# Optimization experiments

Hardware: AMD Instinct MI355X
Metric: run time of the kernel (lower is better)

## Reference

```python
import jax, jax.numpy as jnp
import numpy as np

E, M, K, I, TOPK = 8, 4096, 2048, 1408, 2
N = 2 * I  # gated: w1 produces [gate, up]


def setup_inputs() -> dict:
    key = jax.random.key(0)
    k1, k2, k3, k4, k5 = jax.random.split(key, 5)
    hidden_states = jax.random.normal(k1, (M, K), dtype=jnp.float32)
    w1 = jax.random.normal(k2, (E, N, K), dtype=jnp.float32) * 0.02
    w2 = jax.random.normal(k3, (E, K, I), dtype=jnp.float32) * 0.02
    raw = jax.random.uniform(k4, (M, TOPK), dtype=jnp.float32)
    topk_weights = raw / jnp.sum(raw, axis=-1, keepdims=True)  # router probs
    topk_ids = jax.random.randint(k5, (M, TOPK), 0, E, dtype=jnp.int32)
    return {
        "hidden_states": hidden_states,
        "w1": w1,
        "w2": w2,
        "topk_weights": topk_weights,
        "topk_ids": topk_ids,
    }


def reference(hidden_states, w1, w2, topk_weights, topk_ids):
    # MoE: permute -> grouped GEMM1 -> silu_and_mul -> grouped GEMM2 -> unpermute+reduce.
    # Dense-per-expert formulation (math-equivalent to grouped GEMM over routed tokens).
    # GEMM1: [E, M, N]
    h1 = jnp.einsum("mk,enk->emn", hidden_states, w1)
    gate, up = h1[..., :I], h1[..., I:]
    act = jax.nn.silu(gate) * up  # silu_and_mul, [E, M, I]
    # GEMM2: [E, M, K]
    y = jnp.einsum("emi,eki->emk", act, w2)
    # Unpermute: gather each token's topk expert outputs, apply router weights, reduce.
    y_tok = jnp.transpose(y, (1, 0, 2))  # [M, E, K]
    sel = jnp.take_along_axis(y_tok, topk_ids[:, :, None].astype(jnp.int32), axis=1)  # [M, topk, K]
    out = jnp.sum(sel * topk_weights[:, :, None], axis=1)  # [M, K]
    return out
```

## Files before the change

### kernel.cpp

```cpp
#include <hip/hip_runtime.h>
#include <hip/hip_bf16.h>
#include <stdint.h>

#define EXPERTS 8
#define MTOK 4096
#define KDIM 2048
#define IDIM 1408
#define NDIM 2816
#define CAP  8192

typedef __attribute__((ext_vector_type(8))) short bf16x8;
typedef __attribute__((ext_vector_type(4))) float f32x4;

__device__ __forceinline__ unsigned short f2bf(float x) {
    unsigned u = __float_as_uint(x);
    u = u + 0x7fffu + ((u >> 16) & 1u);
    return (unsigned short)(u >> 16);
}

__device__ __forceinline__ void gload16(const void* g, void* l) {
    __builtin_amdgcn_global_load_lds(
        (const __attribute__((address_space(1))) void*)g,
        (__attribute__((address_space(3))) void*)l, 16, 0, 0);
}

__global__ void __launch_bounds__(256) conv_bf16(const float* __restrict__ src,
                                                 unsigned short* __restrict__ dst, int n4) {
    int i = blockIdx.x * 256 + threadIdx.x;
    int st = gridDim.x * 256;
    for (; i < n4; i += st) {
        float4 v = reinterpret_cast<const float4*>(src)[i];
        ushort4 r;
        r.x = f2bf(v.x); r.y = f2bf(v.y); r.z = f2bf(v.z); r.w = f2bf(v.w);
        reinterpret_cast<ushort4*>(dst)[i] = r;
    }
}

__global__ void __launch_bounds__(256) router(const float* __restrict__ tw,
                                              const int* __restrict__ ids,
                                              int* __restrict__ tok, float* __restrict__ wgt,
                                              int* __restrict__ cnt) {
    int m = blockIdx.x * 256 + threadIdx.x;
    if (m >= MTOK) return;
#pragma unroll
    for (int t = 0; t < 2; t++) {
        int e = ids[m * 2 + t];
        int slot = atomicAdd(&cnt[e], 1);
        tok[e * CAP + slot] = m;
        wgt[e * CAP + slot] = tw[m * 2 + t];
    }
}

__global__ void scan_off(const int* __restrict__ cnt, int* __restrict__ off) {
    if (threadIdx.x == 0) {
        int s = 0;
        for (int e = 0; e < EXPERTS; e++) { off[e] = s; s += cnt[e]; }
    }
}

__global__ void __launch_bounds__(256) gemm1_silu(
    const unsigned short* __restrict__ hsb,
    const unsigned short* __restrict__ w1b,
    const int* __restrict__ tok,
    const int* __restrict__ cnt,
    const int* __restrict__ off,
    unsigned short* __restrict__ act) {
    const int cb = blockIdx.x;
    const int rb = blockIdx.y;
    const int e  = blockIdx.z;
    const int cnt_e = cnt[e];
    if (rb * 128 >= cnt_e) return;
    const int off_e = off[e];

    __shared__ unsigned short As[128 * 32];
    __shared__ unsigned short Bs[128 * 32];
    __shared__ int toks[128];

    const int tid = threadIdx.x;
    const int w = tid >> 6, lane = tid & 63;
    if (tid < 128) {
        int slot = rb * 128 + tid;
        toks[tid] = (slot < cnt_e) ? tok[e * CAP + slot] : 0;
    }
    __syncthreads();

    const int o0 = w * 1024 + lane * 16;
    const int row0 = o0 >> 6, g0 = ((o0 >> 4) & 3) ^ ((row0 >> 1) & 3);
    const int o1 = 4096 + o0;
    const int row1 = o1 >> 6, g1 = ((o1 >> 4) & 3) ^ ((row1 >> 1) & 3);

    const int G0 = row0 >> 4, G1 = row1 >> 4;
    const size_t w1base = (size_t)e * NDIM * KDIM;
    const int wrow0 = ((G0 & 1) ? IDIM : 0) + cb * 64 + (G0 >> 1) * 16 + (row0 & 15);
    const int wrow1 = ((G1 & 1) ? IDIM : 0) + cb * 64 + (G1 >> 1) * 16 + (row1 & 15);

    const int wr = w >> 1, wc = w & 1;
    const int l16 = lane & 15, lg = lane >> 4;

    f32x4 acc[4][4];
#pragma unroll
    for (int m = 0; m < 4; m++)
#pragma unroll
        for (int n = 0; n < 4; n++) acc[m][n] = {0.f, 0.f, 0.f, 0.f};

    char* Ab = (char*)As;
    char* Bb = (char*)Bs;
    const size_t srcA0 = (size_t)toks[row0] * KDIM + g0 * 8;
    const size_t srcA1 = (size_t)toks[row1] * KDIM + g1 * 8;
    const size_t srcB0 = w1base + (size_t)wrow0 * KDIM + g0 * 8;
    const size_t srcB1 = w1base + (size_t)wrow1 * KDIM + g1 * 8;

    for (int kt = 0; kt < KDIM / 32; ++kt) {
        const int kof = kt * 32;
        gload16(hsb + srcA0 + kof, Ab + w * 1024);
        gload16(hsb + srcA1 + kof, Ab + 4096 + w * 1024);
        gload16(w1b + srcB0 + kof, Bb + w * 1024);
        gload16(w1b + srcB1 + kof, Bb + 4096 + w * 1024);
        __syncthreads();

        bf16x8 a[4], b[4];
#pragma unroll
        for (int m = 0; m < 4; m++) {
            int r = wr * 64 + m * 16 + l16;
            a[m] = *reinterpret_cast<bf16x8*>(Ab + r * 64 + ((lg ^ ((r >> 1) & 3)) * 16));
        }
#pragma unroll
        for (int n = 0; n < 4; n++) {
            int r = wc * 64 + n * 16 + l16;
            b[n] = *reinterpret_cast<bf16x8*>(Bb + r * 64 + ((lg ^ ((r >> 1) & 3)) * 16));
        }
#pragma unroll
        for (int m = 0; m < 4; m++)
#pragma unroll
            for (int n = 0; n < 4; n++)
                acc[m][n] = __builtin_amdgcn_mfma_f32_16x16x32_bf16(a[m], b[n], acc[m][n], 0, 0, 0);
        __syncthreads();
    }

#pragma unroll
    for (int m = 0; m < 4; m++) {
#pragma unroll
        for (int np = 0; np < 2; np++) {
            f32x4 g4 = acc[m][np * 2];
            f32x4 u4 = acc[m][np * 2 + 1];
            int icol = cb * 64 + (wc * 2 + np) * 16 + l16;
#pragma unroll
            for (int j = 0; j < 4; j++) {
                int grow = rb * 128 + wr * 64 + m * 16 + lg * 4 + j;
                if (grow < cnt_e) {
                    float gt = g4[j], up = u4[j];
                    float s = gt / (1.f + __expf(-gt));
                    act[(size_t)(off_e + grow) * IDIM + icol] = f2bf(s * up);
                }
            }
        }
    }
}

__global__ void __launch_bounds__(256) gemm2_scatter(
    const unsigned short* __restrict__ act,
    const unsigned short* __restrict__ w2b,
    const int* __restrict__ tok,
    const float* __restrict__ wgt,
    const int* __restrict__ cnt,
    const int* __restrict__ off,
    float* __restrict__ out) {
    const int cb = blockIdx.x;
    const int rb = blockIdx.y;
    const int e  = blockIdx.z;
    const int cnt_e = cnt[e];
    if (rb * 128 >= cnt_e) return;
    const int off_e = off[e];

    __shared__ unsigned short As[128 * 32];
    __shared__ unsigned short Bs[128 * 32];
    __shared__ int toks[128];
    __shared__ float wgts[128];

    const int tid = threadIdx.x;
    const int w = tid >> 6, lane = tid & 63;
    if (tid < 128) {
        int slot = rb * 128 + tid;
        bool v = slot < cnt_e;
        toks[tid] = v ? tok[e * CAP + slot] : 0;
        wgts[tid] = v ? wgt[e * CAP + slot] : 0.f;
    }
    __syncthreads();

    const int o0 = w * 1024 + lane * 16;
    const int row0 = o0 >> 6, g0 = ((o0 >> 4) & 3) ^ ((row0 >> 1) & 3);
    const int o1 = 4096 + o0;
    const int row1 = o1 >> 6, g1 = ((o1 >> 4) & 3) ^ ((row1 >> 1) & 3);

    const int s0 = rb * 128 + row0, s1 = rb * 128 + row1;
    const size_t pa0 = (size_t)(off_e + (s0 < cnt_e ? s0 : 0)) * IDIM + g0 * 8;
    const size_t pa1 = (size_t)(off_e + (s1 < cnt_e ? s1 : 0)) * IDIM + g1 * 8;
    const size_t w2base = (size_t)e * KDIM * IDIM;
    const size_t pb0 = w2base + (size_t)(cb * 128 + row0) * IDIM + g0 * 8;
    const size_t pb1 = w2base + (size_t)(cb * 128 + row1) * IDIM + g1 * 8;

    const int wr = w >> 1, wc = w & 1;
    const int l16 = lane & 15, lg = lane >> 4;

    f32x4 acc[4][4];
#pragma unroll
    for (int m = 0; m < 4; m++)
#pragma unroll
        for (int n = 0; n < 4; n++) acc[m][n] = {0.f, 0.f, 0.f, 0.f};

    char* Ab = (char*)As;
    char* Bb = (char*)Bs;

    for (int kt = 0; kt < IDIM / 32; ++kt) {
        const int kof = kt * 32;
        gload16(act + pa0 + kof, Ab + w * 1024);
        gload16(act + pa1 + kof, Ab + 4096 + w * 1024);
        gload16(w2b + pb0 + kof, Bb + w * 1024);
        gload16(w2b + pb1 + kof, Bb + 4096 + w * 1024);
        __syncthreads();

        bf16x8 a[4], b[4];
#pragma unroll
        for (int m = 0; m < 4; m++) {
            int r = wr * 64 + m * 16 + l16;
            a[m] = *reinterpret_cast<bf16x8*>(Ab + r * 64 + ((lg ^ ((r >> 1) & 3)) * 16));
        }
#pragma unroll
        for (int n = 0; n < 4; n++) {
            int r = wc * 64 + n * 16 + l16;
            b[n] = *reinterpret_cast<bf16x8*>(Bb + r * 64 + ((lg ^ ((r >> 1) & 3)) * 16));
        }
#pragma unroll
        for (int m = 0; m < 4; m++)
#pragma unroll
            for (int n = 0; n < 4; n++)
                acc[m][n] = __builtin_amdgcn_mfma_f32_16x16x32_bf16(a[m], b[n], acc[m][n], 0, 0, 0);
        __syncthreads();
    }

#pragma unroll
    for (int m = 0; m < 4; m++) {
#pragma unroll
        for (int n = 0; n < 4; n++) {
            int kcol = cb * 128 + wc * 64 + n * 16 + l16;
#pragma unroll
            for (int j = 0; j < 4; j++) {
                int lrow = wr * 64 + m * 16 + lg * 4 + j;
                if (rb * 128 + lrow < cnt_e) {
                    atomicAdd(&out[(size_t)toks[lrow] * KDIM + kcol],
                              wgts[lrow] * acc[m][n][j]);
                }
            }
        }
    }
}

extern "C" void kernel_launch(void* const* d_in, const int* in_sizes, int n_in,
                              void* d_out, int out_size, void* d_ws, size_t ws_size,
                              hipStream_t stream) {
    const float* hs  = (const float*)d_in[0];
    const float* w1  = (const float*)d_in[1];
    const float* w2  = (const float*)d_in[2];
    const float* tw  = (const float*)d_in[3];
    const int*   ids = (const int*)d_in[4];
    float* out = (float*)d_out;

    char* ws = (char*)d_ws;
    unsigned short* w1b  = (unsigned short*)(ws);
    unsigned short* w2b  = (unsigned short*)(ws + 92274688ull);
    unsigned short* hsb  = (unsigned short*)(ws + 138412032ull);
    unsigned short* actb = (unsigned short*)(ws + 155189248ull);
    int*   tokb = (int*)  (ws + 178257920ull);
    float* wgtb = (float*)(ws + 178520064ull);
    int*   cntb = (int*)  (ws + 178782208ull);
    int*   offb = (int*)  (ws + 178782240ull);

    hipMemsetAsync(d_out, 0, (size_t)MTOK * KDIM * sizeof(float), stream);
    hipMemsetAsync(cntb, 0, 64, stream);

    conv_bf16<<<4096, 256, 0, stream>>>(w1, w1b, EXPERTS * NDIM * KDIM / 4);
    conv_bf16<<<2048, 256, 0, stream>>>(w2, w2b, EXPERTS * KDIM * IDIM / 4);
    conv_bf16<<<1024, 256, 0, stream>>>(hs, hsb, MTOK * KDIM / 4);

    router<<<MTOK / 256, 256, 0, stream>>>(tw, ids, tokb, wgtb, cntb);
    scan_off<<<1, 64, 0, stream>>>(cntb, offb);

    gemm1_silu<<<dim3(22, 64, 8), 256, 0, stream>>>(hsb, w1b, tokb, cntb, offb, actb);
    gemm2_scatter<<<dim3(16, 64, 8), 256, 0, stream>>>(actb, w2b, tokb, wgtb, cntb, offb, out);
}
```

Before: 400.4 us.

## Enlarge MoE GEMM tiles to 256x256 with a 4-stage async LDS pipeline

Both grouped GEMMs now use 512-thread blocks with 256x256 output tiles and 8 waves, each wave owning a 128x64 sub-tile. Each 32-wide K slice (A and B, 32 KB) is loaded straight into LDS, and a 4-deep ring buffer keeps three slices in flight. Explicit vmcnt waits and a single barrier per step replace the two __syncthreads per step. The MFMA bursts run under raised wave priority. This is meant to hide global-load latency, cut barrier count and raise data reuse per loaded byte. In exchange it uses 128 KB of LDS and more accumulator registers, so occupancy drops to about one block per CU and there are fewer blocks overall.

```diff
diff --git a/kernel.cpp b/kernel.cpp
--- a/kernel.cpp
+++ b/kernel.cpp
@@ -58,7 +58,8 @@
     }
 }
 
-__global__ void __launch_bounds__(256) gemm1_silu(
+
+__global__ void __launch_bounds__(512, 2) gemm1_silu(
     const unsigned short* __restrict__ hsb,
     const unsigned short* __restrict__ w1b,
     const int* __restrict__ tok,
@@ -69,84 +70,105 @@
     const int rb = blockIdx.y;
     const int e  = blockIdx.z;
     const int cnt_e = cnt[e];
-    if (rb * 128 >= cnt_e) return;
+    if (rb * 256 >= cnt_e) return;
     const int off_e = off[e];
-
-    __shared__ unsigned short As[128 * 32];
-    __shared__ unsigned short Bs[128 * 32];
-    __shared__ int toks[128];
+    const int NT = KDIM / 32;
+
+    __shared__ __align__(16) char smem[131072];
+    __shared__ int toks[256];
 
     const int tid = threadIdx.x;
-    const int w = tid >> 6, lane = tid & 63;
-    if (tid < 128) {
-        int slot = rb * 128 + tid;
+    const int lane = tid & 63;
+    const int w = tid >> 6;
+    if (tid < 256) {
+        int slot = rb * 256 + tid;
         toks[tid] = (slot < cnt_e) ? tok[e * CAP + slot] : 0;
     }
     __syncthreads();
 
-    const int o0 = w * 1024 + lane * 16;
-    const int row0 = o0 >> 6, g0 = ((o0 >> 4) & 3) ^ ((row0 >> 1) & 3);
-    const int o1 = 4096 + o0;
-    const int row1 = o1 >> 6, g1 = ((o1 >> 4) & 3) ^ ((row1 >> 1) & 3);
-
-    const int G0 = row0 >> 4, G1 = row1 >> 4;
+    const int offA0 = tid * 16;
+    const int offA1 = 8192 + tid * 16;
+    const int rowA0 = offA0 >> 6, rowA1 = offA1 >> 6;
+    const int gA0 = (tid & 3) ^ ((rowA0 >> 1) & 3);
+    const int gA1 = (tid & 3) ^ ((rowA1 >> 1) & 3);
+    const size_t srcA0 = (size_t)toks[rowA0] * KDIM + gA0 * 8;
+    const size_t srcA1 = (size_t)toks[rowA1] * KDIM + gA1 * 8;
+
     const size_t w1base = (size_t)e * NDIM * KDIM;
-    const int wrow0 = ((G0 & 1) ? IDIM : 0) + cb * 64 + (G0 >> 1) * 16 + (row0 & 15);
-    const int wrow1 = ((G1 & 1) ? IDIM : 0) + cb * 64 + (G1 >> 1) * 16 + (row1 & 15);
-
-    const int wr = w >> 1, wc = w & 1;
+    const int G0 = rowA0 >> 4, G1 = rowA1 >> 4;
+    const int w1row0 = ((G0 & 1) ? IDIM : 0) + cb * 128 + (G0 >> 1) * 16 + (rowA0 & 15);
+    const int w1row1 = ((G1 & 1) ? IDIM : 0) + cb * 128 + (G1 >> 1) * 16 + (rowA1 & 15);
+    const size_t srcB0 = w1base + (size_t)w1row0 * KDIM + gA0 * 8;
+    const size_t srcB1 = w1base + (size_t)w1row1 * KDIM + gA1 * 8;
+
+    const int wr = w >> 2, wc = w & 3;
     const int l16 = lane & 15, lg = lane >> 4;
 
-    f32x4 acc[4][4];
-#pragma unroll
-    for (int m = 0; m < 4; m++)
+    f32x4 acc[8][4];
+#pragma unroll
+    for (int m = 0; m < 8; m++)
 #pragma unroll
         for (int n = 0; n < 4; n++) acc[m][n] = {0.f, 0.f, 0.f, 0.f};
 
-    char* Ab = (char*)As;
-    char* Bb = (char*)Bs;
-    const size_t srcA0 = (size_t)toks[row0] * KDIM + g0 * 8;
-    const size_t srcA1 = (size_t)toks[row1] * KDIM + g1 * 8;
-    const size_t srcB0 = w1base + (size_t)wrow0 * KDIM + g0 * 8;
-    const size_t srcB1 = w1base + (size_t)wrow1 * KDIM + g1 * 8;
-
-    for (int kt = 0; kt < KDIM / 32; ++kt) {
-        const int kof = kt * 32;
-        gload16(hsb + srcA0 + kof, Ab + w * 1024);
-        gload16(hsb + srcA1 + kof, Ab + 4096 + w * 1024);
-        gload16(w1b + srcB0 + kof, Bb + w * 1024);
-        gload16(w1b + srcB1 + kof, Bb + 4096 + w * 1024);
-        __syncthreads();
-
-        bf16x8 a[4], b[4];
-#pragma unroll
-        for (int m = 0; m < 4; m++) {
-            int r = wr * 64 + m * 16 + l16;
-            a[m] = *reinterpret_cast<bf16x8*>(Ab + r * 64 + ((lg ^ ((r >> 1) & 3)) * 16));
-        }
+#define STAGE1(s) { \
+    char* sb_ = smem + (((s) & 3) << 15); \
+    const int kof_ = (s) * 32; \
+    gload16(hsb + srcA0 + kof_, sb_ + tid * 16); \
+    gload16(hsb + srcA1 + kof_, sb_ + 8192 + tid * 16); \
+    gload16(w1b + srcB0 + kof_, sb_ + 16384 + tid * 16); \
+    gload16(w1b + srcB1 + kof_, sb_ + 24576 + tid * 16); }
+
+    STAGE1(0); STAGE1(1); STAGE1(2);
+    asm volatile("s_waitcnt vmcnt(8)");
+    __builtin_amdgcn_sched_barrier(0);
+    asm volatile("s_barrier" ::: "memory");
+    __builtin_amdgcn_sched_barrier(0);
+
+    for (int t = 0; t < NT; ++t) {
+        char* db = smem + ((t & 3) << 15);
+        if (t + 3 < NT) STAGE1(t + 3);
+
+        bf16x8 b[4];
 #pragma unroll
         for (int n = 0; n < 4; n++) {
             int r = wc * 64 + n * 16 + l16;
-            b[n] = *reinterpret_cast<bf16x8*>(Bb + r * 64 + ((lg ^ ((r >> 1) & 3)) * 16));
-        }
-#pragma unroll
-        for (int m = 0; m < 4; m++)
-#pragma unroll
-            for (int n = 0; n < 4; n++)
-                acc[m][n] = __builtin_amdgcn_mfma_f32_16x16x32_bf16(a[m], b[n], acc[m][n], 0, 0, 0);
-        __syncthreads();
-    }
-
-#pragma unroll
-    for (int m = 0; m < 4; m++) {
-#pragma unroll
-        for (int np = 0; np < 2; np++) {
-            f32x4 g4 = acc[m][np * 2];
-            f32x4 u4 = acc[m][np * 2 + 1];
-            int icol = cb * 64 + (wc * 2 + np) * 16 + l16;
+            b[n] = *reinterpret_cast<bf16x8*>(db + 16384 + r * 64 + ((lg ^ ((r >> 1) & 3)) * 16));
+        }
+#pragma unroll
+        for (int q = 0; q < 4; q++) {
+            int r0 = wr * 128 + (2 * q) * 16 + l16;
+            int r1 = r0 + 16;
+            bf16x8 a0 = *reinterpret_cast<bf16x8*>(db + r0 * 64 + ((lg ^ ((r0 >> 1) & 3)) * 16));
+            bf16x8 a1 = *reinterpret_cast<bf16x8*>(db + r1 * 64 + ((lg ^ ((r1 >> 1) & 3)) * 16));
+            __builtin_amdgcn_s_setprio(1);
+#pragma unroll
+            for (int n = 0; n < 4; n++) {
+                acc[2 * q][n]     = __builtin_amdgcn_mfma_f32_16x16x32_bf16(a0, b[n], acc[2 * q][n], 0, 0, 0);
+                acc[2 * q + 1][n] = __builtin_amdgcn_mfma_f32_16x16x32_bf16(a1, b[n], acc[2 * q + 1][n], 0, 0, 0);
+            }
+            __builtin_amdgcn_s_setprio(0);
+        }
+        __builtin_amdgcn_sched_barrier(0);
+        if (t + 1 < NT) {
+            if (t + 3 < NT)      { asm volatile("s_waitcnt vmcnt(8)"); }
+            else if (t + 2 < NT) { asm volatile("s_waitcnt vmcnt(4)"); }
+            else                 { asm volatile("s_waitcnt vmcnt(0)"); }
+            asm volatile("s_barrier" ::: "memory");
+            __builtin_amdgcn_sched_barrier(0);
+        }
+    }
+#undef STAGE1
+
+#pragma unroll
+    for (int m = 0; m < 8; m++) {
+#pragma unroll
+        for (int p = 0; p < 2; p++) {
+            f32x4 g4 = acc[m][p * 2];
+            f32x4 u4 = acc[m][p * 2 + 1];
+            int icol = cb * 128 + (wc * 2 + p) * 16 + l16;
 #pragma unroll
             for (int j = 0; j < 4; j++) {
-                int grow = rb * 128 + wr * 64 + m * 16 + lg * 4 + j;
+                int grow = rb * 256 + wr * 128 + m * 16 + lg * 4 + j;
                 if (grow < cnt_e) {
                     float gt = g4[j], up = u4[j];
                     float s = gt / (1.f + __expf(-gt));
@@ -157,7 +179,7 @@
     }
 }
 
-__global__ void __launch_bounds__(256) gemm2_scatter(
+__global__ void __launch_bounds__(512, 2) gemm2_scatter(
     const unsigned short* __restrict__ act,
     const unsigned short* __restrict__ w2b,
     const int* __restrict__ tok,
@@ -169,84 +191,105 @@
     const int rb = blockIdx.y;
     const int e  = blockIdx.z;
     const int cnt_e = cnt[e];
-    if (rb * 128 >= cnt_e) return;
+    if (rb * 256 >= cnt_e) return;
     const int off_e = off[e];
-
-    __shared__ unsigned short As[128 * 32];
-    __shared__ unsigned short Bs[128 * 32];
-    __shared__ int toks[128];
-    __shared__ float wgts[128];
+    const int NT = IDIM / 32;
+
+    __shared__ __align__(16) char smem[131072];
+    __shared__ int toks[256];
+    __shared__ float wgts[256];
 
     const int tid = threadIdx.x;
-    const int w = tid >> 6, lane = tid & 63;
-    if (tid < 128) {
-        int slot = rb * 128 + tid;
+    const int lane = tid & 63;
+    const int w = tid >> 6;
+    if (tid < 256) {
+        int slot = rb * 256 + tid;
         bool v = slot < cnt_e;
         toks[tid] = v ? tok[e * CAP + slot] : 0;
         wgts[tid] = v ? wgt[e * CAP + slot] : 0.f;
     }
     __syncthreads();
 
-    const int o0 = w * 1024 + lane * 16;
-    const int row0 = o0 >> 6, g0 = ((o0 >> 4) & 3) ^ ((row0 >> 1) & 3);
-    const int o1 = 4096 + o0;
-    const int row1 = o1 >> 6, g1 = ((o1 >> 4) & 3) ^ ((row1 >> 1) & 3);
-
-    const int s0 = rb * 128 + row0, s1 = rb * 128 + row1;
-    const size_t pa0 = (size_t)(off_e + (s0 < cnt_e ? s0 : 0)) * IDIM + g0 * 8;
-    const size_t pa1 = (size_t)(off_e + (s1 < cnt_e ? s1 : 0)) * IDIM + g1 * 8;
+    const int offA0 = tid * 16;
+    const int offA1 = 8192 + tid * 16;
+    const int rowA0 = offA0 >> 6, rowA1 = offA1 >> 6;
+    const int gA0 = (tid & 3) ^ ((rowA0 >> 1) & 3);
+    const int gA1 = (tid & 3) ^ ((rowA1 >> 1) & 3);
+    const int s0 = rb * 256 + rowA0, s1 = rb * 256 + rowA1;
+    const size_t srcA0 = (size_t)(off_e + (s0 < cnt_e ? s0 : 0)) * IDIM + gA0 * 8;
+    const size_t srcA1 = (size_t)(off_e + (s1 < cnt_e ? s1 : 0)) * IDIM + gA1 * 8;
+
     const size_t w2base = (size_t)e * KDIM * IDIM;
-    const size_t pb0 = w2base + (size_t)(cb * 128 + row0) * IDIM + g0 * 8;
-    const size_t pb1 = w2base + (size_t)(cb * 128 + row1) * IDIM + g1 * 8;
-
-    const int wr = w >> 1, wc = w & 1;
+    const size_t srcB0 = w2base + (size_t)(cb * 256 + rowA0) * IDIM + gA0 * 8;
+    const size_t srcB1 = w2base + (size_t)(cb * 256 + rowA1) * IDIM + gA1 * 8;
+
+    const int wr = w >> 2, wc = w & 3;
     const int l16 = lane & 15, lg = lane >> 4;
 
-    f32x4 acc[4][4];
-#pragma unroll
-    for (int m = 0; m < 4; m++)
+    f32x4 acc[8][4];
+#pragma unroll
+    for (int m = 0; m < 8; m++)
 #pragma unroll
         for (int n = 0; n < 4; n++) acc[m][n] = {0.f, 0.f, 0.f, 0.f};
 
-    char* Ab = (char*)As;
-    char* Bb = (char*)Bs;
-
-    for (int kt = 0; kt < IDIM / 32; ++kt) {
-        const int kof = kt * 32;
-        gload16(act + pa0 + kof, Ab + w * 1024);
-        gload16(act + pa1 + kof, Ab + 4096 + w * 1024);
-        gload16(w2b + pb0 + kof, Bb + w * 1024);
-        gload16(w2b + pb1 + kof, Bb + 4096 + w * 1024);
-        __syncthreads();
-
-        bf16x8 a[4], b[4];
-#pragma unroll
-        for (int m = 0; m < 4; m++) {
-            int r = wr * 64 + m * 16 + l16;
-            a[m] = *reinterpret_cast<bf16x8*>(Ab + r * 64 + ((lg ^ ((r >> 1) & 3)) * 16));
-        }
+#define STAGE2(s) { \
+    char* sb_ = smem + (((s) & 3) << 15); \
+    const int kof_ = (s) * 32; \
+    gload16(act + srcA0 + kof_, sb_ + tid * 16); \
+    gload16(act + srcA1 + kof_, sb_ + 8192 + tid * 16); \
+    gload16(w2b + srcB0 + kof_, sb_ + 16384 + tid * 16); \
+    gload16(w2b + srcB1 + kof_, sb_ + 24576 + tid * 16); }
+
+    STAGE2(0); STAGE2(1); STAGE2(2);
+    asm volatile("s_waitcnt vmcnt(8)");
+    __builtin_amdgcn_sched_barrier(0);
+    asm volatile("s_barrier" ::: "memory");
+    __builtin_amdgcn_sched_barrier(0);
+
+    for (int t = 0; t < NT; ++t) {
+        char* db = smem + ((t & 3) << 15);
+        if (t + 3 < NT) STAGE2(t + 3);
+
+        bf16x8 b[4];
 #pragma unroll
         for (int n = 0; n < 4; n++) {
             int r = wc * 64 + n * 16 + l16;
-            b[n] = *reinterpret_cast<bf16x8*>(Bb + r * 64 + ((lg ^ ((r >> 1) & 3)) * 16));
-        }
-#pragma unroll
-        for (int m = 0; m < 4; m++)
-#pragma unroll
-            for (int n = 0; n < 4; n++)
-                acc[m][n] = __builtin_amdgcn_mfma_f32_16x16x32_bf16(a[m], b[n], acc[m][n], 0, 0, 0);
-        __syncthreads();
-    }
-
-#pragma unroll
-    for (int m = 0; m < 4; m++) {
+            b[n] = *reinterpret_cast<bf16x8*>(db + 16384 + r * 64 + ((lg ^ ((r >> 1) & 3)) * 16));
+        }
+#pragma unroll
+        for (int q = 0; q < 4; q++) {
+            int r0 = wr * 128 + (2 * q) * 16 + l16;
+            int r1 = r0 + 16;
+            bf16x8 a0 = *reinterpret_cast<bf16x8*>(db + r0 * 64 + ((lg ^ ((r0 >> 1) & 3)) * 16));
+            bf16x8 a1 = *reinterpret_cast<bf16x8*>(db + r1 * 64 + ((lg ^ ((r1 >> 1) & 3)) * 16));
+            __builtin_amdgcn_s_setprio(1);
+#pragma unroll
+            for (int n = 0; n < 4; n++) {
+                acc[2 * q][n]     = __builtin_amdgcn_mfma_f32_16x16x32_bf16(a0, b[n], acc[2 * q][n], 0, 0, 0);
+                acc[2 * q + 1][n] = __builtin_amdgcn_mfma_f32_16x16x32_bf16(a1, b[n], acc[2 * q + 1][n], 0, 0, 0);
+            }
+            __builtin_amdgcn_s_setprio(0);
+        }
+        __builtin_amdgcn_sched_barrier(0);
+        if (t + 1 < NT) {
+            if (t + 3 < NT)      { asm volatile("s_waitcnt vmcnt(8)"); }
+            else if (t + 2 < NT) { asm volatile("s_waitcnt vmcnt(4)"); }
+            else                 { asm volatile("s_waitcnt vmcnt(0)"); }
+            asm volatile("s_barrier" ::: "memory");
+            __builtin_amdgcn_sched_barrier(0);
+        }
+    }
+#undef STAGE2
+
+#pragma unroll
+    for (int m = 0; m < 8; m++) {
 #pragma unroll
         for (int n = 0; n < 4; n++) {
-            int kcol = cb * 128 + wc * 64 + n * 16 + l16;
+            int kcol = cb * 256 + wc * 64 + n * 16 + l16;
 #pragma unroll
             for (int j = 0; j < 4; j++) {
-                int lrow = wr * 64 + m * 16 + lg * 4 + j;
-                if (rb * 128 + lrow < cnt_e) {
+                int lrow = wr * 128 + m * 16 + lg * 4 + j;
+                if (rb * 256 + lrow < cnt_e) {
                     atomicAdd(&out[(size_t)toks[lrow] * KDIM + kcol],
                               wgts[lrow] * acc[m][n][j]);
                 }
@@ -285,6 +328,6 @@
     router<<<MTOK / 256, 256, 0, stream>>>(tw, ids, tokb, wgtb, cntb);
     scan_off<<<1, 64, 0, stream>>>(cntb, offb);
 
-    gemm1_silu<<<dim3(22, 64, 8), 256, 0, stream>>>(hsb, w1b, tokb, cntb, offb, actb);
-    gemm2_scatter<<<dim3(16, 64, 8), 256, 0, stream>>>(actb, w2b, tokb, wgtb, cntb, offb, out);
-}
+    gemm1_silu<<<dim3(11, 32, 8), 512, 0, stream>>>(hsb, w1b, tokb, cntb, offb, actb);
+    gemm2_scatter<<<dim3(8, 32, 8), 512, 0, stream>>>(actb, w2b, tokb, wgtb, cntb, offb, out);
+}
```

After: 451.7 us. +12.8%, slower.

## Triple-buffer gemm1 with 128x256 tiles, 512 threads and interleaved MFMA/load schedule

Applied to the files above, without the earlier changes.

Rewrites the gated GEMM1 kernel to use a 128x256 output tile over 8 waves with a K step of 64. Three LDS stages of 48KB each prefetch two tiles ahead, and the global-to-LDS loads are spread between the four MFMA sub-phases using explicit barriers, waitcnt and setprio. An 8-way XOR swizzle is meant to avoid bank conflicts. The goal is to hide memory latency and raise MFMA utilisation. In exchange the kernel needs 147KB of LDS, which limits occupancy to one block per CU, and hand-tuned vmcnt counts make it fragile.

```diff
diff --git a/kernel.cpp b/kernel.cpp
--- a/kernel.cpp
+++ b/kernel.cpp
@@ -58,7 +58,7 @@
     }
 }
 
-__global__ void __launch_bounds__(256) gemm1_silu(
+__global__ void __launch_bounds__(512, 2) gemm1_silu(
     const unsigned short* __restrict__ hsb,
     const unsigned short* __restrict__ w1b,
     const int* __restrict__ tok,
@@ -71,31 +71,57 @@
     const int cnt_e = cnt[e];
     if (rb * 128 >= cnt_e) return;
     const int off_e = off[e];
-
-    __shared__ unsigned short As[128 * 32];
-    __shared__ unsigned short Bs[128 * 32];
+    const int NT = KDIM / 64;
+
+    __shared__ __align__(16) char smem[147456];
     __shared__ int toks[128];
 
     const int tid = threadIdx.x;
-    const int w = tid >> 6, lane = tid & 63;
+    const int lane = tid & 63;
+    const int w = tid >> 6;
     if (tid < 128) {
         int slot = rb * 128 + tid;
         toks[tid] = (slot < cnt_e) ? tok[e * CAP + slot] : 0;
     }
     __syncthreads();
 
-    const int o0 = w * 1024 + lane * 16;
-    const int row0 = o0 >> 6, g0 = ((o0 >> 4) & 3) ^ ((row0 >> 1) & 3);
-    const int o1 = 4096 + o0;
-    const int row1 = o1 >> 6, g1 = ((o1 >> 4) & 3) ^ ((row1 >> 1) & 3);
-
-    const int G0 = row0 >> 4, G1 = row1 >> 4;
-    const size_t w1base = (size_t)e * NDIM * KDIM;
-    const int wrow0 = ((G0 & 1) ? IDIM : 0) + cb * 64 + (G0 >> 1) * 16 + (row0 & 15);
-    const int wrow1 = ((G1 & 1) ? IDIM : 0) + cb * 64 + (G1 >> 1) * 16 + (row1 & 15);
-
-    const int wr = w >> 1, wc = w & 1;
+    size_t sA[2]; int dA[2];
+#pragma unroll
+    for (int c = 0; c < 2; c++) {
+        int i = c * 512 + tid;
+        int row = i >> 3, gp = i & 7, gl = gp ^ (row & 7);
+        sA[c] = (size_t)toks[row] * KDIM + gl * 8;
+        dA[c] = i * 16;
+    }
+    size_t sB[4]; int dB[4];
+    const size_t w1base = (size_t)e * (size_t)NDIM * KDIM;
+#pragma unroll
+    for (int c = 0; c < 4; c++) {
+        int j = c * 512 + tid;
+        int row = j >> 3, gp = j & 7, gl = gp ^ (row & 7);
+        int G = row >> 4;
+        int w1row = ((G & 1) ? IDIM : 0) + cb * 128 + (G >> 1) * 16 + (row & 15);
+        sB[c] = w1base + (size_t)w1row * KDIM + gl * 8;
+        dB[c] = 16384 + j * 16;
+    }
+
+    const int wr = w >> 2, wc = w & 3;
     const int l16 = lane & 15, lg = lane >> 4;
+    int aoff[4][2], boff[4][2];
+#pragma unroll
+    for (int m = 0; m < 4; m++) {
+        int row = wr * 64 + m * 16 + l16;
+#pragma unroll
+        for (int h = 0; h < 2; h++)
+            aoff[m][h] = row * 128 + (((h * 4 + lg) ^ (row & 7)) * 16);
+    }
+#pragma unroll
+    for (int n = 0; n < 4; n++) {
+        int row = wc * 64 + n * 16 + l16;
+#pragma unroll
+        for (int h = 0; h < 2; h++)
+            boff[n][h] = 16384 + row * 128 + (((h * 4 + lg) ^ (row & 7)) * 16);
+    }
 
     f32x4 acc[4][4];
 #pragma unroll
@@ -103,47 +129,115 @@
 #pragma unroll
         for (int n = 0; n < 4; n++) acc[m][n] = {0.f, 0.f, 0.f, 0.f};
 
-    char* Ab = (char*)As;
-    char* Bb = (char*)Bs;
-    const size_t srcA0 = (size_t)toks[row0] * KDIM + g0 * 8;
-    const size_t srcA1 = (size_t)toks[row1] * KDIM + g1 * 8;
-    const size_t srcB0 = w1base + (size_t)wrow0 * KDIM + g0 * 8;
-    const size_t srcB1 = w1base + (size_t)wrow1 * KDIM + g1 * 8;
-
-    for (int kt = 0; kt < KDIM / 32; ++kt) {
-        const int kof = kt * 32;
-        gload16(hsb + srcA0 + kof, Ab + w * 1024);
-        gload16(hsb + srcA1 + kof, Ab + 4096 + w * 1024);
-        gload16(w1b + srcB0 + kof, Bb + w * 1024);
-        gload16(w1b + srcB1 + kof, Bb + 4096 + w * 1024);
-        __syncthreads();
-
-        bf16x8 a[4], b[4];
-#pragma unroll
-        for (int m = 0; m < 4; m++) {
-            int r = wr * 64 + m * 16 + l16;
-            a[m] = *reinterpret_cast<bf16x8*>(Ab + r * 64 + ((lg ^ ((r >> 1) & 3)) * 16));
-        }
+#define STG_A(t, base) { const int ko_ = (t) * 64; \
+    gload16(hsb + sA[0] + ko_, (base) + dA[0]); \
+    gload16(hsb + sA[1] + ko_, (base) + dA[1]); }
+#define STG_B01(t, base) { const int ko_ = (t) * 64; \
+    gload16(w1b + sB[0] + ko_, (base) + dB[0]); \
+    gload16(w1b + sB[1] + ko_, (base) + dB[1]); }
+#define STG_B23(t, base) { const int ko_ = (t) * 64; \
+    gload16(w1b + sB[2] + ko_, (base) + dB[2]); \
+    gload16(w1b + sB[3] + ko_, (base) + dB[3]); }
+
+    STG_A(0, smem); STG_B01(0, smem); STG_B23(0, smem);
+    { char* s1 = smem + 49152; STG_A(1, s1); STG_B01(1, s1); STG_B23(1, s1); }
+    asm volatile("s_waitcnt vmcnt(6)" ::: "memory");
+    __builtin_amdgcn_sched_barrier(0);
+    __builtin_amdgcn_s_barrier();
+
+    int cb_o = 0;
+    int st_o = 98304;
+
+#pragma unroll 1
+    for (int t = 0; t < NT; ++t) {
+        char* db = smem + cb_o;
+        char* sb = smem + st_o;
+        const bool stg = (t + 2 < NT);
+        const int ko = (t + 2) * 64;
+
+        bf16x8 bv0[4], bv1[4];
 #pragma unroll
         for (int n = 0; n < 4; n++) {
-            int r = wc * 64 + n * 16 + l16;
-            b[n] = *reinterpret_cast<bf16x8*>(Bb + r * 64 + ((lg ^ ((r >> 1) & 3)) * 16));
-        }
-#pragma unroll
-        for (int m = 0; m < 4; m++)
-#pragma unroll
-            for (int n = 0; n < 4; n++)
-                acc[m][n] = __builtin_amdgcn_mfma_f32_16x16x32_bf16(a[m], b[n], acc[m][n], 0, 0, 0);
-        __syncthreads();
-    }
+            bv0[n] = *(const bf16x8*)(db + boff[n][0]);
+            bv1[n] = *(const bf16x8*)(db + boff[n][1]);
+        }
+        bf16x8 a0 = *(const bf16x8*)(db + aoff[0][0]);
+        bf16x8 a1 = *(const bf16x8*)(db + aoff[0][1]);
+        if (stg) { gload16(hsb + sA[0] + ko, sb + dA[0]); gload16(hsb + sA[1] + ko, sb + dA[1]); }
+        __builtin_amdgcn_sched_barrier(0);
+        __builtin_amdgcn_s_barrier();
+        asm volatile("s_waitcnt lgkmcnt(0)" ::: "memory");
+        __builtin_amdgcn_sched_barrier(0);
+        __builtin_amdgcn_s_setprio(1);
+#pragma unroll
+        for (int n = 0; n < 4; n++) acc[0][n] = __builtin_amdgcn_mfma_f32_16x16x32_bf16(a0, bv0[n], acc[0][n], 0, 0, 0);
+#pragma unroll
+        for (int n = 0; n < 4; n++) acc[0][n] = __builtin_amdgcn_mfma_f32_16x16x32_bf16(a1, bv1[n], acc[0][n], 0, 0, 0);
+        __builtin_amdgcn_s_setprio(0);
+        __builtin_amdgcn_sched_barrier(0);
+
+        a0 = *(const bf16x8*)(db + aoff[1][0]);
+        a1 = *(const bf16x8*)(db + aoff[1][1]);
+        if (stg) { gload16(w1b + sB[0] + ko, sb + dB[0]); gload16(w1b + sB[1] + ko, sb + dB[1]); }
+        __builtin_amdgcn_sched_barrier(0);
+        __builtin_amdgcn_s_barrier();
+        asm volatile("s_waitcnt lgkmcnt(0)" ::: "memory");
+        __builtin_amdgcn_sched_barrier(0);
+        __builtin_amdgcn_s_setprio(1);
+#pragma unroll
+        for (int n = 0; n < 4; n++) acc[1][n] = __builtin_amdgcn_mfma_f32_16x16x32_bf16(a0, bv0[n], acc[1][n], 0, 0, 0);
+#pragma unroll
+        for (int n = 0; n < 4; n++) acc[1][n] = __builtin_amdgcn_mfma_f32_16x16x32_bf16(a1, bv1[n], acc[1][n], 0, 0, 0);
+        __builtin_amdgcn_s_setprio(0);
+        __builtin_amdgcn_sched_barrier(0);
+
+        a0 = *(const bf16x8*)(db + aoff[2][0]);
+        a1 = *(const bf16x8*)(db + aoff[2][1]);
+        if (stg) { gload16(w1b + sB[2] + ko, sb + dB[2]); gload16(w1b + sB[3] + ko, sb + dB[3]); }
+        __builtin_amdgcn_sched_barrier(0);
+        __builtin_amdgcn_s_barrier();
+        asm volatile("s_waitcnt lgkmcnt(0)" ::: "memory");
+        __builtin_amdgcn_sched_barrier(0);
+        __builtin_amdgcn_s_setprio(1);
+#pragma unroll
+        for (int n = 0; n < 4; n++) acc[2][n] = __builtin_amdgcn_mfma_f32_16x16x32_bf16(a0, bv0[n], acc[2][n], 0, 0, 0);
+#pragma unroll
+        for (int n = 0; n < 4; n++) acc[2][n] = __builtin_amdgcn_mfma_f32_16x16x32_bf16(a1, bv1[n], acc[2][n], 0, 0, 0);
+        __builtin_amdgcn_s_setprio(0);
+        __builtin_amdgcn_sched_barrier(0);
+
+        a0 = *(const bf16x8*)(db + aoff[3][0]);
+        a1 = *(const bf16x8*)(db + aoff[3][1]);
+        __builtin_amdgcn_sched_barrier(0);
+        __builtin_amdgcn_s_barrier();
+        asm volatile("s_waitcnt lgkmcnt(0)" ::: "memory");
+        __builtin_amdgcn_sched_barrier(0);
+        __builtin_amdgcn_s_setprio(1);
+#pragma unroll
+        for (int n = 0; n < 4; n++) acc[3][n] = __builtin_amdgcn_mfma_f32_16x16x32_bf16(a0, bv0[n], acc[3][n], 0, 0, 0);
+#pragma unroll
+        for (int n = 0; n < 4; n++) acc[3][n] = __builtin_amdgcn_mfma_f32_16x16x32_bf16(a1, bv1[n], acc[3][n], 0, 0, 0);
+        __builtin_amdgcn_s_setprio(0);
+        __builtin_amdgcn_sched_barrier(0);
+        if (t + 2 < NT)      { asm volatile("s_waitcnt vmcnt(6)" ::: "memory"); }
+        else if (t + 1 < NT) { asm volatile("s_waitcnt vmcnt(0)" ::: "memory"); }
+        __builtin_amdgcn_sched_barrier(0);
+        __builtin_amdgcn_s_barrier();
+
+        cb_o += 49152; if (cb_o == 147456) cb_o = 0;
+        st_o += 49152; if (st_o == 147456) st_o = 0;
+    }
+#undef STG_A
+#undef STG_B01
+#undef STG_B23
 
 #pragma unroll
     for (int m = 0; m < 4; m++) {
 #pragma unroll
-        for (int np = 0; np < 2; np++) {
-            f32x4 g4 = acc[m][np * 2];
-            f32x4 u4 = acc[m][np * 2 + 1];
-            int icol = cb * 64 + (wc * 2 + np) * 16 + l16;
+        for (int p = 0; p < 2; p++) {
+            f32x4 g4 = acc[m][p * 2];
+            f32x4 u4 = acc[m][p * 2 + 1];
+            int icol = cb * 128 + (wc * 2 + p) * 16 + l16;
 #pragma unroll
             for (int j = 0; j < 4; j++) {
                 int grow = rb * 128 + wr * 64 + m * 16 + lg * 4 + j;
@@ -285,6 +379,6 @@
     router<<<MTOK / 256, 256, 0, stream>>>(tw, ids, tokb, wgtb, cntb);
     scan_off<<<1, 64, 0, stream>>>(cntb, offb);
 
-    gemm1_silu<<<dim3(22, 64, 8), 256, 0, stream>>>(hsb, w1b, tokb, cntb, offb, actb);
+    gemm1_silu<<<dim3(11, 64, 8), 512, 0, stream>>>(hsb, w1b, tokb, cntb, offb, actb);
     gemm2_scatter<<<dim3(16, 64, 8), 256, 0, stream>>>(actb, w2b, tokb, wgtb, cntb, offb, out);
 }
```

Measured after the change: 464.3 us. 16.0% more time.
